# Optimization experiments

Hardware: AMD Instinct MI355X
Metric: run time of the kernel (lower is better)

The kernel has to match this reference:

```python
import jax, jax.numpy as jnp
import numpy as np

N = 50000      # nodes
E = 800000     # top-down edges (before self-loops)
IN = 256       # in_dim
HID = 64       # hidden_dim
H = 4          # heads
SLOPE = 0.2    # PyG GATConv leaky_relu negative_slope


def setup_inputs() -> dict:
    key = jax.random.key(0)
    ks = jax.random.split(key, 12)
    g = lambda k, s, fan: jax.random.normal(k, s, dtype=jnp.float32) / np.float32(np.sqrt(fan))
    return {
        "x": jax.random.normal(ks[0], (N, IN), dtype=jnp.float32),
        "root_features": jax.random.normal(ks[1], (N, IN), dtype=jnp.float32),
        "edge_index": jax.random.randint(ks[2], (2, E), 0, N, dtype=jnp.int32),
        "W1": g(ks[3], (H * HID, IN), IN),
        "a_src1": g(ks[4], (H, HID), HID),
        "a_dst1": g(ks[5], (H, HID), HID),
        "b1": jnp.zeros((H * HID,), jnp.float32),
        "W2": g(ks[6], (H * HID, H * HID), H * HID),
        "a_src2": g(ks[7], (H, HID), HID),
        "a_dst2": g(ks[8], (H, HID), HID),
        "b2": jnp.zeros((HID,), jnp.float32),
        "Wr": g(ks[9], (HID, IN), IN),
        "br": jnp.zeros((HID,), jnp.float32),
    }


def gat_conv(h_in, src, dst, W, a_src, a_dst, bias, concat):
    """PyG GATConv (eval mode): gather -> attention logit -> segment softmax -> scatter."""
    h = (h_in @ W.T).reshape(-1, H, HID)                 # [N, H, C]
    alpha_s = jnp.einsum('nhc,hc->nh', h, a_src)         # [N, H]
    alpha_d = jnp.einsum('nhc,hc->nh', h, a_dst)
    logits = jax.nn.leaky_relu(alpha_s[src] + alpha_d[dst], SLOPE)   # [Etot, H]
    # numerically stable softmax over incoming edges of each dst node
    m = jax.ops.segment_max(logits, dst, num_segments=N)             # [N, H]
    e = jnp.exp(logits - m[dst])
    denom = jax.ops.segment_sum(e, dst, num_segments=N)              # [N, H]
    alpha = e / denom[dst]                                           # self-loops => denom > 0
    out = jax.ops.segment_sum(alpha[:, :, None] * h[src], dst, num_segments=N)  # [N, H, C]
    if concat:
        return out.reshape(-1, H * HID) + bias
    return out.mean(axis=1) + bias


def reference(x, root_features, edge_index, W1, a_src1, a_dst1, b1,
              W2, a_src2, a_dst2, b2, Wr, br):
    # PyG GATConv adds self-loops by default
    loops = jnp.arange(N, dtype=edge_index.dtype)
    src = jnp.concatenate([edge_index[0], loops])   # parents (message sources)
    dst = jnp.concatenate([edge_index[1], loops])   # children (aggregation targets)

    h = gat_conv(x, src, dst, W1, a_src1, a_dst1, b1, concat=True)   # [N, H*HID]
    h = jax.nn.relu(h)                                               # dropout = identity in eval
    h = gat_conv(h, src, dst, W2, a_src2, a_dst2, b2, concat=False)  # [N, HID]
    return h + root_features @ Wr.T + br
```

## Files before the change

### kernel.cpp

```cpp
#include <hip/hip_runtime.h>
#include <hip/hip_bf16.h>
#include <math.h>

#define NN   50000
#define EE   800000
#define ETOT (EE + NN)
#define KDIM 256
#define HEADS 4
#define HIDD 64
#define DCAP 64

typedef float  f32x4  __attribute__((ext_vector_type(4)));
typedef short  bf16x8 __attribute__((ext_vector_type(8)));

__device__ __forceinline__ float b2f(unsigned short u) {
    union { float f; unsigned int i; } v; v.i = (unsigned int)u << 16; return v.f;
}
__device__ __forceinline__ unsigned short f2b(float f) {
    union { float f; unsigned int i; } v; v.f = f;
    return (unsigned short)((v.i + 0x7fffu + ((v.i >> 16) & 1u)) >> 16);
}
__device__ __forceinline__ float lrelu(float x) { return x >= 0.f ? x : 0.2f * x; }

#define CASTB 144
#define PREPB (CASTB + (NN + 255) / 256)

__global__ __launch_bounds__(256) void prep_k(
    const float* __restrict__ W1, const float* __restrict__ W2,
    const float* __restrict__ Wr, unsigned short* __restrict__ wout,
    int* __restrict__ deg)
{
    int b = blockIdx.x;
    if (b < CASTB) {
        int i = (b * 256 + threadIdx.x) * 4;
        const float* src;
        int off;
        if (i < 65536)        { src = W1; off = 0; }
        else if (i < 131072)  { src = W2; off = 65536; }
        else                  { src = Wr; off = 131072; }
        float4 v = *reinterpret_cast<const float4*>(src + (i - off));
        ushort4 o;
        o.x = f2b(v.x); o.y = f2b(v.y); o.z = f2b(v.z); o.w = f2b(v.w);
        *reinterpret_cast<ushort4*>(wout + i) = o;
    } else {
        int i = (b - CASTB) * 256 + threadIdx.x;
        if (i < NN) deg[i] = 0;
    }
}

__global__ __launch_bounds__(256) void fill64_k(
    const int* __restrict__ ei, int* __restrict__ deg, int* __restrict__ EDG)
{
    int e = blockIdx.x * 256 + threadIdx.x;
    if (e >= ETOT) return;
    int src, dst;
    if (e < EE) { src = ei[e]; dst = ei[EE + e]; }
    else        { src = dst = e - EE; }
    int pos = atomicAdd(deg + dst, 1) & (DCAP - 1);
    EDG[(size_t)dst * DCAP + pos] = src;
}

template<bool AF32, int NCT, bool ALPHA, bool OUTF32>
__global__ __launch_bounds__(256) void gemm_mfma(
    const void* __restrict__ Ain, const unsigned short* __restrict__ W,
    void* __restrict__ Cout, int Mrows,
    const float* __restrict__ av_src, const float* __restrict__ av_dst,
    float* __restrict__ AS, float* __restrict__ AD,
    const float* __restrict__ bias0, const float* __restrict__ bias1)
{
    constexpr int ROWS = NCT * 16;
    constexpr int KS   = 32;
    constexpr int LDK  = 40;
    constexpr int NSL  = KDIM / KS;
    constexpr int NLD  = (ROWS * KS) / (256 * 8);
    __shared__ unsigned short Wl[2][ROWS][LDK];

    const int t    = threadIdx.x;
    const int wid  = t >> 6;
    const int lane = t & 63;
    const int cl   = lane & 15;
    const int kg   = lane >> 4;
    const int m0   = (blockIdx.x * 4 + wid) * 16;

    int arow = m0 + cl; if (arow >= Mrows) arow = Mrows - 1;

    bf16x8 stg[NLD];
    auto LOADSTG = [&](int s) {
        #pragma unroll
        for (int i = 0; i < NLD; i++) {
            int f = i * 256 + t;
            int c = f >> 2, kc = f & 3;
            stg[i] = *reinterpret_cast<const bf16x8*>(
                W + (size_t)c * KDIM + s * KS + kc * 8);
        }
    };
    auto WRITESTG = [&](int b) {
        #pragma unroll
        for (int i = 0; i < NLD; i++) {
            int f = i * 256 + t;
            int c = f >> 2, kc = f & 3;
            *reinterpret_cast<bf16x8*>(&Wl[b][c][kc * 8]) = stg[i];
        }
    };
    auto LOADA = [&](int s) -> bf16x8 {
        if constexpr (AF32) {
            const float* ap = (const float*)Ain + (size_t)arow * KDIM + s * KS + kg * 8;
            float4 v0 = *reinterpret_cast<const float4*>(ap);
            float4 v1 = *reinterpret_cast<const float4*>(ap + 4);
            bf16x8 a;
            a[0] = (short)f2b(v0.x); a[1] = (short)f2b(v0.y);
            a[2] = (short)f2b(v0.z); a[3] = (short)f2b(v0.w);
            a[4] = (short)f2b(v1.x); a[5] = (short)f2b(v1.y);
            a[6] = (short)f2b(v1.z); a[7] = (short)f2b(v1.w);
            return a;
        } else {
            return *reinterpret_cast<const bf16x8*>(
                (const unsigned short*)Ain + (size_t)arow * KDIM + s * KS + kg * 8);
        }
    };

    f32x4 acc[NCT];
    #pragma unroll
    for (int ct = 0; ct < NCT; ct++) acc[ct] = (f32x4)(0.f);

    LOADSTG(0);
    WRITESTG(0);
    bf16x8 a_cur = LOADA(0);
    __syncthreads();

    int buf = 0;
    for (int s = 0; s < NSL; s++) {
        bf16x8 a_nxt;
        if (s + 1 < NSL) { LOADSTG(s + 1); a_nxt = LOADA(s + 1); }
        #pragma unroll
        for (int ct = 0; ct < NCT; ct++) {
            bf16x8 b = *reinterpret_cast<const bf16x8*>(&Wl[buf][ct * 16 + cl][kg * 8]);
            acc[ct] = __builtin_amdgcn_mfma_f32_16x16x32_bf16(a_cur, b, acc[ct], 0, 0, 0);
        }
        if (s + 1 < NSL) {
            WRITESTG(buf ^ 1);
            __syncthreads();
            buf ^= 1;
            a_cur = a_nxt;
        }
    }

    if constexpr (OUTF32) {
        float* C = (float*)Cout;
        #pragma unroll
        for (int ct = 0; ct < NCT; ct++) {
            #pragma unroll
            for (int r = 0; r < 4; r++) {
                int n = m0 + kg * 4 + r;
                int c = ct * 16 + cl;
                if (n < Mrows)
                    C[(size_t)n * (NCT * 16) + c] = acc[ct][r] + bias0[c] + bias1[c];
            }
        }
    } else {
        unsigned short* C = (unsigned short*)Cout;
        #pragma unroll
        for (int ct = 0; ct < NCT; ct++) {
            #pragma unroll
            for (int r = 0; r < 4; r++) {
                int n = m0 + kg * 4 + r;
                if (n < Mrows)
                    C[(size_t)n * (NCT * 16) + ct * 16 + cl] = f2b(acc[ct][r]);
            }
        }
    }

    if constexpr (ALPHA) {
        float asr[NCT], adr[NCT];
        #pragma unroll
        for (int ct = 0; ct < NCT; ct++) {
            int c = ct * 16 + cl;
            asr[ct] = av_src[c];
            adr[ct] = av_dst[c];
        }
        #pragma unroll
        for (int r = 0; r < 4; r++) {
            int n = m0 + kg * 4 + r;
            f32x4 s4 = (f32x4)(0.f), d4 = (f32x4)(0.f);
            #pragma unroll
            for (int h = 0; h < 4; h++) {
                #pragma unroll
                for (int q = 0; q < 4; q++) {
                    s4[h] += acc[h * 4 + q][r] * asr[h * 4 + q];
                    d4[h] += acc[h * 4 + q][r] * adr[h * 4 + q];
                }
            }
            #pragma unroll
            for (int msk = 1; msk <= 8; msk <<= 1) {
                #pragma unroll
                for (int h = 0; h < 4; h++) {
                    s4[h] += __shfl_xor(s4[h], msk, 64);
                    d4[h] += __shfl_xor(d4[h], msk, 64);
                }
            }
            if (cl == 0 && n < Mrows) {
                *reinterpret_cast<float4*>(AS + (size_t)n * 4) =
                    make_float4(s4[0], s4[1], s4[2], s4[3]);
                *reinterpret_cast<float4*>(AD + (size_t)n * 4) =
                    make_float4(d4[0], d4[1], d4[2], d4[3]);
            }
        }
    }
}

template<int MODE>
__global__ __launch_bounds__(256) void gather_k(
    const int* __restrict__ deg, const int* __restrict__ EDG,
    const float* __restrict__ AS, const float* __restrict__ AD,
    const unsigned short* __restrict__ H, const float* __restrict__ bias,
    unsigned short* __restrict__ OUT, float* __restrict__ OUTF)
{
    __shared__ float wT[4][4][65];
    int wid  = threadIdx.x >> 6;
    int lane = threadIdx.x & 63;
    int n = blockIdx.x * 4 + wid;
    if (n >= NN) return;
    int head = lane >> 4;

    int cd = min(deg[n], DCAP);
    float4 ad4 = *reinterpret_cast<const float4*>(AD + (size_t)n * 4);

    int srcv = (lane < cd) ? EDG[(size_t)n * DCAP + lane] : 0;
    float4 w4 = make_float4(0.f, 0.f, 0.f, 0.f);
    if (lane < cd) {
        float4 s4 = *reinterpret_cast<const float4*>(AS + (size_t)srcv * 4);
        w4.x = __expf(lrelu(s4.x + ad4.x));
        w4.y = __expf(lrelu(s4.y + ad4.y));
        w4.z = __expf(lrelu(s4.z + ad4.z));
        w4.w = __expf(lrelu(s4.w + ad4.w));
    }
    wT[wid][0][lane] = w4.x;
    wT[wid][1][lane] = w4.y;
    wT[wid][2][lane] = w4.z;
    wT[wid][3][lane] = w4.w;

    float4 den4 = w4;
    #pragma unroll
    for (int msk = 1; msk <= 32; msk <<= 1) {
        den4.x += __shfl_xor(den4.x, msk, 64);
        den4.y += __shfl_xor(den4.y, msk, 64);
        den4.z += __shfl_xor(den4.z, msk, 64);
        den4.w += __shfl_xor(den4.w, msk, 64);
    }
    float den = head == 0 ? den4.x : head == 1 ? den4.y : head == 2 ? den4.z : den4.w;
    float inv = 1.f / den;

    float a0 = 0.f, a1 = 0.f, a2 = 0.f, a3 = 0.f;
    float c0 = 0.f, c1 = 0.f, c2 = 0.f, c3 = 0.f;
    const unsigned short* hp = H + lane * 4;

    int j = 0;
    for (; j + 4 <= cd; j += 4) {
        int   sA = __builtin_amdgcn_readlane(srcv, j);
        int   sB = __builtin_amdgcn_readlane(srcv, j + 1);
        int   sC = __builtin_amdgcn_readlane(srcv, j + 2);
        int   sD = __builtin_amdgcn_readlane(srcv, j + 3);
        float wA = wT[wid][head][j];
        float wB = wT[wid][head][j + 1];
        float wC = wT[wid][head][j + 2];
        float wD = wT[wid][head][j + 3];
        ushort4 hA = *reinterpret_cast<const ushort4*>(hp + (size_t)sA * 256);
        ushort4 hB = *reinterpret_cast<const ushort4*>(hp + (size_t)sB * 256);
        ushort4 hC = *reinterpret_cast<const ushort4*>(hp + (size_t)sC * 256);
        ushort4 hD = *reinterpret_cast<const ushort4*>(hp + (size_t)sD * 256);
        a0 += wA * b2f(hA.x); a1 += wA * b2f(hA.y);
        a2 += wA * b2f(hA.z); a3 += wA * b2f(hA.w);
        c0 += wB * b2f(hB.x); c1 += wB * b2f(hB.y);
        c2 += wB * b2f(hB.z); c3 += wB * b2f(hB.w);
        a0 += wC * b2f(hC.x); a1 += wC * b2f(hC.y);
        a2 += wC * b2f(hC.z); a3 += wC * b2f(hC.w);
        c0 += wD * b2f(hD.x); c1 += wD * b2f(hD.y);
        c2 += wD * b2f(hD.z); c3 += wD * b2f(hD.w);
    }
    for (; j < cd; j++) {
        int   sA = __builtin_amdgcn_readlane(srcv, j);
        float wA = wT[wid][head][j];
        ushort4 hA = *reinterpret_cast<const ushort4*>(hp + (size_t)sA * 256);
        a0 += wA * b2f(hA.x); a1 += wA * b2f(hA.y);
        a2 += wA * b2f(hA.z); a3 += wA * b2f(hA.w);
    }
    a0 += c0; a1 += c1; a2 += c2; a3 += c3;

    if (MODE == 1) {
        float4 bv = *reinterpret_cast<const float4*>(bias + lane * 4);
        ushort4 o;
        o.x = f2b(fmaxf(a0 * inv + bv.x, 0.f));
        o.y = f2b(fmaxf(a1 * inv + bv.y, 0.f));
        o.z = f2b(fmaxf(a2 * inv + bv.z, 0.f));
        o.w = f2b(fmaxf(a3 * inv + bv.w, 0.f));
        *reinterpret_cast<ushort4*>(OUT + (size_t)n * 256 + lane * 4) = o;
    } else {
        float v0 = a0 * inv, v1 = a1 * inv, v2 = a2 * inv, v3 = a3 * inv;
        #pragma unroll
        for (int msk = 16; msk <= 32; msk <<= 1) {
            v0 += __shfl_xor(v0, msk, 64);
            v1 += __shfl_xor(v1, msk, 64);
            v2 += __shfl_xor(v2, msk, 64);
            v3 += __shfl_xor(v3, msk, 64);
        }
        if (lane < 16) {
            float4* o = reinterpret_cast<float4*>(OUTF + (size_t)n * 64 + lane * 4);
            float4 cur = *o;
            cur.x += 0.25f * v0;
            cur.y += 0.25f * v1;
            cur.z += 0.25f * v2;
            cur.w += 0.25f * v3;
            *o = cur;
        }
    }
}

extern "C" void kernel_launch(void* const* d_in, const int* in_sizes, int n_in,
                              void* d_out, int out_size, void* d_ws, size_t ws_size,
                              hipStream_t stream) {
    const float* x    = (const float*)d_in[0];
    const float* root = (const float*)d_in[1];
    const int*   ei   = (const int*)  d_in[2];
    const float* W1   = (const float*)d_in[3];
    const float* as1  = (const float*)d_in[4];
    const float* ad1  = (const float*)d_in[5];
    const float* b1   = (const float*)d_in[6];
    const float* W2   = (const float*)d_in[7];
    const float* as2  = (const float*)d_in[8];
    const float* ad2  = (const float*)d_in[9];
    const float* b2   = (const float*)d_in[10];
    const float* Wr   = (const float*)d_in[11];
    const float* br   = (const float*)d_in[12];
    float* out = (float*)d_out;

    unsigned short* Hb  = (unsigned short*)d_ws;
    unsigned short* X2b = Hb  + (size_t)NN * 256;
    unsigned short* w1b = X2b + (size_t)NN * 256;
    unsigned short* w2b = w1b + 65536;
    unsigned short* wrb = w2b + 65536;
    float* AS  = (float*)(wrb + 16384);
    float* AD  = AS + (size_t)NN * 4;
    int*   deg = (int*)(AD + (size_t)NN * 4);
    int*   EDG = deg + NN;

    const int egrid = (ETOT + 255) / 256;
    const int wgrid = (NN + 3) / 4;
    const int mgrid = (NN + 63) / 64;

    prep_k<<<PREPB, 256, 0, stream>>>(W1, W2, Wr, w1b, deg);

    fill64_k<<<egrid, 256, 0, stream>>>(ei, deg, EDG);

    gemm_mfma<true, 16, true, false><<<mgrid, 256, 0, stream>>>(
        x, w1b, Hb, NN, as1, ad1, AS, AD, nullptr, nullptr);
    gather_k<1><<<wgrid, 256, 0, stream>>>(deg, EDG, AS, AD, Hb, b1, X2b, nullptr);

    gemm_mfma<false, 16, true, false><<<mgrid, 256, 0, stream>>>(
        X2b, w2b, Hb, NN, as2, ad2, AS, AD, nullptr, nullptr);

    gemm_mfma<true, 4, false, true><<<mgrid, 256, 0, stream>>>(
        root, wrb, out, NN, nullptr, nullptr, nullptr, nullptr, br, b2);
    gather_k<2><<<wgrid, 256, 0, stream>>>(deg, EDG, AS, AD, Hb, nullptr, nullptr, out);
}
```

Before: 255.1 us.

## Fuse layer-1 GEMM, root GEMM and edge bucketing into one kernel launch

Merges the layer-1 feature GEMM, the root-feature GEMM and the edge-bucketing atomic fill into a single kernel that picks its role from the block index, so these independent stages run side by side. Degree zeroing moves to hipMemsetAsync and the weight cast kernel is trimmed to match. This cuts launch count and lets the memory-bound atomic fill overlap the MFMA GEMMs. In exchange, every block reserves the full 40 KB of shared memory, including the small-tile GEMM and fill blocks, which may lower occupancy for those roles.

After: 257.9 us. No clear change (+1.1%).

```diff
diff --git a/kernel.cpp b/kernel.cpp
--- a/kernel.cpp
+++ b/kernel.cpp
@@ -23,45 +23,26 @@
 __device__ __forceinline__ float lrelu(float x) { return x >= 0.f ? x : 0.2f * x; }
 
 #define CASTB 144
-#define PREPB (CASTB + (NN + 255) / 256)
 
 __global__ __launch_bounds__(256) void prep_k(
     const float* __restrict__ W1, const float* __restrict__ W2,
-    const float* __restrict__ Wr, unsigned short* __restrict__ wout,
-    int* __restrict__ deg)
-{
-    int b = blockIdx.x;
-    if (b < CASTB) {
-        int i = (b * 256 + threadIdx.x) * 4;
-        const float* src;
-        int off;
-        if (i < 65536)        { src = W1; off = 0; }
-        else if (i < 131072)  { src = W2; off = 65536; }
-        else                  { src = Wr; off = 131072; }
-        float4 v = *reinterpret_cast<const float4*>(src + (i - off));
-        ushort4 o;
-        o.x = f2b(v.x); o.y = f2b(v.y); o.z = f2b(v.z); o.w = f2b(v.w);
-        *reinterpret_cast<ushort4*>(wout + i) = o;
-    } else {
-        int i = (b - CASTB) * 256 + threadIdx.x;
-        if (i < NN) deg[i] = 0;
-    }
-}
-
-__global__ __launch_bounds__(256) void fill64_k(
-    const int* __restrict__ ei, int* __restrict__ deg, int* __restrict__ EDG)
-{
-    int e = blockIdx.x * 256 + threadIdx.x;
-    if (e >= ETOT) return;
-    int src, dst;
-    if (e < EE) { src = ei[e]; dst = ei[EE + e]; }
-    else        { src = dst = e - EE; }
-    int pos = atomicAdd(deg + dst, 1) & (DCAP - 1);
-    EDG[(size_t)dst * DCAP + pos] = src;
+    const float* __restrict__ Wr, unsigned short* __restrict__ wout)
+{
+    int i = (blockIdx.x * 256 + threadIdx.x) * 4;
+    const float* src;
+    int off;
+    if (i < 65536)        { src = W1; off = 0; }
+    else if (i < 131072)  { src = W2; off = 65536; }
+    else                  { src = Wr; off = 131072; }
+    float4 v = *reinterpret_cast<const float4*>(src + (i - off));
+    ushort4 o;
+    o.x = f2b(v.x); o.y = f2b(v.y); o.z = f2b(v.z); o.w = f2b(v.w);
+    *reinterpret_cast<ushort4*>(wout + i) = o;
 }
 
 template<bool AF32, int NCT, bool ALPHA, bool OUTF32>
-__global__ __launch_bounds__(256) void gemm_mfma(
+__device__ __forceinline__ void gemm_body(
+    unsigned short* __restrict__ WlRaw, int bid,
     const void* __restrict__ Ain, const unsigned short* __restrict__ W,
     void* __restrict__ Cout, int Mrows,
     const float* __restrict__ av_src, const float* __restrict__ av_dst,
@@ -73,14 +54,13 @@
     constexpr int LDK  = 40;
     constexpr int NSL  = KDIM / KS;
     constexpr int NLD  = (ROWS * KS) / (256 * 8);
-    __shared__ unsigned short Wl[2][ROWS][LDK];
 
     const int t    = threadIdx.x;
     const int wid  = t >> 6;
     const int lane = t & 63;
     const int cl   = lane & 15;
     const int kg   = lane >> 4;
-    const int m0   = (blockIdx.x * 4 + wid) * 16;
+    const int m0   = (bid * 4 + wid) * 16;
 
     int arow = m0 + cl; if (arow >= Mrows) arow = Mrows - 1;
 
@@ -99,7 +79,7 @@
         for (int i = 0; i < NLD; i++) {
             int f = i * 256 + t;
             int c = f >> 2, kc = f & 3;
-            *reinterpret_cast<bf16x8*>(&Wl[b][c][kc * 8]) = stg[i];
+            *reinterpret_cast<bf16x8*>(&WlRaw[(size_t)(b * ROWS + c) * LDK + kc * 8]) = stg[i];
         }
     };
     auto LOADA = [&](int s) -> bf16x8 {
@@ -134,7 +114,8 @@
         if (s + 1 < NSL) { LOADSTG(s + 1); a_nxt = LOADA(s + 1); }
         #pragma unroll
         for (int ct = 0; ct < NCT; ct++) {
-            bf16x8 b = *reinterpret_cast<const bf16x8*>(&Wl[buf][ct * 16 + cl][kg * 8]);
+            bf16x8 b = *reinterpret_cast<const bf16x8*>(
+                &WlRaw[(size_t)(buf * ROWS + ct * 16 + cl) * LDK + kg * 8]);
             acc[ct] = __builtin_amdgcn_mfma_f32_16x16x32_bf16(a_cur, b, acc[ct], 0, 0, 0);
         }
         if (s + 1 < NSL) {
@@ -206,6 +187,49 @@
             }
         }
     }
+}
+
+#define MG ((NN + 63) / 64)
+#define EG ((ETOT + 255) / 256)
+
+__global__ __launch_bounds__(256) void mega1_k(
+    const float* __restrict__ x, const unsigned short* __restrict__ w1b,
+    unsigned short* __restrict__ Hb,
+    const float* __restrict__ as1, const float* __restrict__ ad1,
+    float* __restrict__ AS, float* __restrict__ AD,
+    const float* __restrict__ root, const unsigned short* __restrict__ wrb,
+    float* __restrict__ out, const float* __restrict__ br, const float* __restrict__ b2,
+    const int* __restrict__ ei, int* __restrict__ deg, int* __restrict__ EDG)
+{
+    __shared__ unsigned short Wl[2 * 256 * 40];
+    int b = blockIdx.x;
+    if (b < MG) {
+        gemm_body<true, 16, true, false>(Wl, b, x, w1b, Hb, NN,
+                                         as1, ad1, AS, AD, nullptr, nullptr);
+    } else if (b < 2 * MG) {
+        gemm_body<true, 4, false, true>(Wl, b - MG, root, wrb, out, NN,
+                                        nullptr, nullptr, nullptr, nullptr, br, b2);
+    } else {
+        int e = (b - 2 * MG) * 256 + threadIdx.x;
+        if (e < ETOT) {
+            int src, dst;
+            if (e < EE) { src = ei[e]; dst = ei[EE + e]; }
+            else        { src = dst = e - EE; }
+            int pos = atomicAdd(deg + dst, 1) & (DCAP - 1);
+            EDG[(size_t)dst * DCAP + pos] = src;
+        }
+    }
+}
+
+__global__ __launch_bounds__(256) void gemm2_k(
+    const unsigned short* __restrict__ X2b, const unsigned short* __restrict__ w2b,
+    unsigned short* __restrict__ Hb,
+    const float* __restrict__ as2, const float* __restrict__ ad2,
+    float* __restrict__ AS, float* __restrict__ AD)
+{
+    __shared__ unsigned short Wl[2 * 256 * 40];
+    gemm_body<false, 16, true, false>(Wl, blockIdx.x, X2b, w2b, Hb, NN,
+                                      as2, ad2, AS, AD, nullptr, nullptr);
 }
 
 template<int MODE>
@@ -343,22 +367,16 @@
     int*   deg = (int*)(AD + (size_t)NN * 4);
     int*   EDG = deg + NN;
 
-    const int egrid = (ETOT + 255) / 256;
     const int wgrid = (NN + 3) / 4;
-    const int mgrid = (NN + 63) / 64;
-
-    prep_k<<<PREPB, 256, 0, stream>>>(W1, W2, Wr, w1b, deg);
-
-    fill64_k<<<egrid, 256, 0, stream>>>(ei, deg, EDG);
-
-    gemm_mfma<true, 16, true, false><<<mgrid, 256, 0, stream>>>(
-        x, w1b, Hb, NN, as1, ad1, AS, AD, nullptr, nullptr);
+
+    hipMemsetAsync(deg, 0, NN * sizeof(int), stream);
+    prep_k<<<CASTB, 256, 0, stream>>>(W1, W2, Wr, w1b);
+
+    mega1_k<<<2 * MG + EG, 256, 0, stream>>>(x, w1b, Hb, as1, ad1, AS, AD,
+                                             root, wrb, out, br, b2,
+                                             ei, deg, EDG);
     gather_k<1><<<wgrid, 256, 0, stream>>>(deg, EDG, AS, AD, Hb, b1, X2b, nullptr);
 
-    gemm_mfma<false, 16, true, false><<<mgrid, 256, 0, stream>>>(
-        X2b, w2b, Hb, NN, as2, ad2, AS, AD, nullptr, nullptr);
-
-    gemm_mfma<true, 4, false, true><<<mgrid, 256, 0, stream>>>(
-        root, wrb, out, NN, nullptr, nullptr, nullptr, nullptr, br, b2);
+    gemm2_k<<<MG, 256, 0, stream>>>(X2b, w2b, Hb, as2, ad2, AS, AD);
     gather_k<2><<<wgrid, 256, 0, stream>>>(deg, EDG, AS, AD, Hb, nullptr, nullptr, out);
 }
```
